# Performance work log

Hardware: AMD Instinct MI355X
Metric: run time of the kernel (lower is better)

The kernel has to match this reference:

```python
import jax, jax.numpy as jnp
import numpy as np

BATCH = 64
EPS = 1e-5
SLOPE = 0.2


def setup_inputs() -> dict:
    key = jax.random.key(0)
    ks = jax.random.split(key, 12)
    def n(k, shape, scale=0.05):
        return jax.random.normal(k, shape, dtype=jnp.float32) * scale
    inp = {"x": jax.random.normal(ks[0], (BATCH, 3, 64, 768), dtype=jnp.float32)}
    depths = [(3, 16), (16, 32), (32, 64), (64, 128), (128, 256)]
    for i, (ci, co) in enumerate(depths):
        inp[f"w{i}"] = n(ks[1 + i], (co, ci, 4, 4))
        inp[f"g{i}"] = jnp.ones((co,), jnp.float32)
        inp[f"b{i}"] = jnp.zeros((co,), jnp.float32)
    inp["w5"] = n(ks[10], (1000, 256, 2, 2))
    inp["lin_w"] = n(ks[11], (64, 1000))
    return inp


def _conv(x, w, s, p):
    return jax.lax.conv_general_dilated(
        x, w, (s, s), ((p, p), (p, p)),
        dimension_numbers=("NCHW", "OIHW", "NCHW"))


def _bn(x, g, b):
    # training-mode BatchNorm2d: batch statistics over (N, H, W)
    m = jnp.mean(x, axis=(0, 2, 3), keepdims=True)
    v = jnp.var(x, axis=(0, 2, 3), keepdims=True)
    return (x - m) * jax.lax.rsqrt(v + EPS) * g[None, :, None, None] + b[None, :, None, None]


def _leaky(x):
    return jnp.where(x >= 0, x, SLOPE * x)


def reference(x, w0, g0, b0, w1, g1, b1, w2, g2, b2, w3, g3, b3, w4, g4, b4, w5, lin_w):
    for w, g, b in [(w0, g0, b0), (w1, g1, b1), (w2, g2, b2), (w3, g3, b3), (w4, g4, b4)]:
        x = _leaky(_bn(_conv(x, w, 2, 1), g, b))
    x = _conv(x, w5, 1, 0)                      # [B, 1000, 1, 23]
    B = x.shape[0]
    sub = x.reshape(B, 1000, -1)                # [B, 1000, 23]
    sub = _leaky(sub)                           # per-slice LeakyReLU == elementwise
    sub = jnp.einsum('bcj,oc->boj', sub, lin_w)  # batched per-slice Linear, fused
    sub = jax.nn.sigmoid(sub)                   # [B, 64, 23]
    a = sub[:, :32, :]                          # low half
    bh = sub[:, 32:, :]                         # high half
    mid = (bh[:, :, :22] + a[:, :, 1:]) * 0.5   # j = 1..22 blend
    small = jnp.concatenate([a[:, :, :1], mid, bh[:, :, 22:]], axis=2)  # [B, 32, 24]
    # torch.cat over dim=1 of small[:,:,j] for j=0..23 -> j-major layout
    return jnp.transpose(small, (0, 2, 1)).reshape(B, 32 * 24)
```

## Files before the change

### kernel.cpp

```cpp
#include <hip/hip_runtime.h>
#include <cmath>

#define EPS 1e-5f
#define SLOPE 0.2f

typedef unsigned short u16;
typedef unsigned int u32;
typedef __attribute__((ext_vector_type(8))) short bf16x8;
typedef __attribute__((ext_vector_type(8))) unsigned short u16x8;
typedef __attribute__((ext_vector_type(4))) unsigned short u16x4;
typedef __attribute__((ext_vector_type(4))) float f32x4;

__device__ __forceinline__ u16 f2b(float f) {
    union { float f; u32 u; } v; v.f = f;
    u32 r = (v.u + 0x7FFF + ((v.u >> 16) & 1)) >> 16;
    return (u16)r;
}
__device__ __forceinline__ float b2f(u16 h) {
    union { u32 u; float f; } v; v.u = ((u32)h) << 16;
    return v.f;
}
__device__ __forceinline__ float leaky(float v) { return v >= 0.f ? v : SLOPE * v; }

__global__ __launch_bounds__(256) void prep(const float* __restrict__ x,
                                            const float* __restrict__ w0,
                                            const float* __restrict__ w1,
                                            const float* __restrict__ w2,
                                            const float* __restrict__ w3,
                                            const float* __restrict__ w4,
                                            const float* __restrict__ w5,
                                            const float* __restrict__ lw,
                                            u16* __restrict__ wbf,
                                            u16* __restrict__ w5b,
                                            u16* __restrict__ lwb,
                                            u16* __restrict__ P) {
    int idx = blockIdx.x * 256 + threadIdx.x;
    if (idx < 697344) {
        const float* src; int K, lgn, base;
        if (idx < 1024)        { src = w0; K = 48;   lgn = 1; base = 0; }
        else if (idx < 9216)   { src = w1; K = 256;  lgn = 3; base = 1024; }
        else if (idx < 41984)  { src = w2; K = 512;  lgn = 4; base = 9216; }
        else if (idx < 173056) { src = w3; K = 1024; lgn = 5; base = 41984; }
        else                   { src = w4; K = 2048; lgn = 6; base = 173056; }
        int local = idx - base;
        int e = local & 7;
        int r = (local >> 3) & 15;
        int q = (local >> 7) & 3;
        int rest = local >> 9;
        int kb = rest & ((1 << lgn) - 1);
        int tm = rest >> lgn;
        int co = tm * 16 + r;
        int k  = kb * 32 + q * 8 + e;
        wbf[idx] = (k < K) ? f2b(src[(size_t)co * K + k]) : (u16)0;
    } else if (idx < 1745920) {
        int local = idx - 697344;
        int k = local & 1023;
        int co = local >> 10;
        w5b[local] = (co < 1000) ? f2b(w5[(size_t)co * 1024 + k]) : (u16)0;
    } else if (idx < 1811456) {
        int local = idx - 1745920;
        int e = local & 7;
        int r = (local >> 3) & 15;
        int q = (local >> 7) & 3;
        int rest = local >> 9;
        int kb = rest & 31;
        int tm = rest >> 5;
        int o = tm * 16 + r;
        int k = kb * 32 + q * 8 + e;
        lwb[local] = (k < 1000) ? f2b(lw[(size_t)o * 1000 + k]) : (u16)0;
    } else if (idx < 3450368) {
        constexpr int H = 64, W = 768, G = 97, Wp = 776, Hp = 66;
        int local = idx - 1811456;
        int m = local % G;
        int hp = (local / G) % Hp;
        int c = (local / (G * Hp)) % 4;
        int b = local / (G * Hp * 4);
        u16x8 o;
#pragma unroll
        for (int i = 0; i < 8; ++i) o[i] = 0;
        if (c < 3 && hp >= 1 && hp <= H) {
            const float* base = x + ((size_t)(b * 3 + c) * H + (hp - 1)) * W;
            if (m > 0) o[0] = f2b(base[8 * m - 1]);
            if (m < G - 1) {
                float4 a  = *(const float4*)(base + 8 * m);
                float4 b4 = *(const float4*)(base + 8 * m + 4);
                o[1] = f2b(a.x); o[2] = f2b(a.y); o[3] = f2b(a.z); o[4] = f2b(a.w);
                o[5] = f2b(b4.x); o[6] = f2b(b4.y); o[7] = f2b(b4.z);
            }
        }
        *(u16x8*)(P + ((size_t)(b * 4 + c) * Hp + hp) * Wp + 8 * m) = o;
    }
}

template <int Co, int CiPad, int Kp, int Hi, int Wi, int Hp, int Wp, int MT, int NT>
__global__ __launch_bounds__(256) void conv_mfma(const u16* __restrict__ inp,
                                                 const u16* __restrict__ wt,
                                                 u16* __restrict__ outb,
                                                 float* __restrict__ part) {
    constexpr int Ho = Hi / 2, Wo = Wi / 2, HW = Ho * Wo;
    constexpr int NTile = 4 * HW;
    constexpr int NG = NTile / NT;
    constexpr int NSLOT = NG / 4;

    int tid = threadIdx.x;
    int wv = tid >> 6;
    int wid = blockIdx.x * 4 + wv;
    int lane = tid & 63;
    int r = lane & 15;
    int quad = lane >> 4;
    int mg = wid / NG;
    int ng = wid % NG;

    int ciq = quad >> 1;
    int kh0 = (quad & 1) * 2;

    const u16* pB[NT];
    int b_[NT], hw_[NT];
#pragma unroll
    for (int i = 0; i < NT; ++i) {
        int n = (ng * NT + i) * 16 + r;
        int b = n / HW;
        int hw = n % HW;
        int oh = hw / Wo;
        int ow = hw % Wo;
        b_[i] = b; hw_[i] = hw;
        pB[i] = inp + ((size_t)(b * CiPad + ciq) * Hp + (2 * oh + kh0)) * Wp + 2 * ow;
    }
    const u16* pA = wt + (size_t)(mg * MT) * 16 * Kp + quad * 128 + r * 8;

    f32x4 acc[MT][NT];
#pragma unroll
    for (int mt = 0; mt < MT; ++mt)
#pragma unroll
        for (int i = 0; i < NT; ++i) acc[mt][i] = (f32x4){0.f, 0.f, 0.f, 0.f};

#pragma unroll 2
    for (int kk = 0; kk < Kp / 32; ++kk) {
        bf16x8 a[MT];
#pragma unroll
        for (int mt = 0; mt < MT; ++mt)
            a[mt] = *(const bf16x8*)(pA + (size_t)mt * 16 * Kp);
#pragma unroll
        for (int i = 0; i < NT; ++i) {
            union { u32 u[4]; bf16x8 v; } bb;
            bb.u[0] = *(const u32*)(pB[i]);
            bb.u[1] = *(const u32*)(pB[i] + 2);
            bb.u[2] = *(const u32*)(pB[i] + Wp);
            bb.u[3] = *(const u32*)(pB[i] + Wp + 2);
#pragma unroll
            for (int mt = 0; mt < MT; ++mt)
                acc[mt][i] = __builtin_amdgcn_mfma_f32_16x16x32_bf16(a[mt], bb.v, acc[mt][i], 0, 0, 0);
            pB[i] += (size_t)2 * Hp * Wp;
        }
        pA += 512;
    }

#pragma unroll
    for (int mt = 0; mt < MT; ++mt) {
        int co0 = mg * MT * 16 + mt * 16 + quad * 4;
#pragma unroll
        for (int i = 0; i < NT; ++i) {
#pragma unroll
            for (int j = 0; j < 4; ++j)
                outb[((size_t)b_[i] * Co + co0 + j) * HW + hw_[i]] = f2b(acc[mt][i][j]);
        }
    }

    __shared__ float sred[4][MT * 16 * 2];
#pragma unroll
    for (int mt = 0; mt < MT; ++mt) {
#pragma unroll
        for (int j = 0; j < 4; ++j) {
            float ls1 = 0.f, ls2 = 0.f;
#pragma unroll
            for (int i = 0; i < NT; ++i) {
                float v = acc[mt][i][j];
                ls1 += v; ls2 += v * v;
            }
#pragma unroll
            for (int m = 1; m < 16; m <<= 1) {
                ls1 += __shfl_xor(ls1, m);
                ls2 += __shfl_xor(ls2, m);
            }
            if (r == 0) {
                int cl = mt * 16 + quad * 4 + j;
                sred[wv][cl * 2 + 0] = ls1;
                sred[wv][cl * 2 + 1] = ls2;
            }
        }
    }
    __syncthreads();
    int slot = blockIdx.x % NSLOT;
    int mgb  = blockIdx.x / NSLOT;
    if (tid < MT * 16) {
        float s1 = (sred[0][tid * 2] + sred[1][tid * 2]) +
                   (sred[2][tid * 2] + sred[3][tid * 2]);
        float s2 = (sred[0][tid * 2 + 1] + sred[1][tid * 2 + 1]) +
                   (sred[2][tid * 2 + 1] + sred[3][tid * 2 + 1]);
        part[((size_t)(mgb * MT * 16 + tid) * NSLOT + slot) * 2 + 0] = s1;
        part[((size_t)(mgb * MT * 16 + tid) * NSLOT + slot) * 2 + 1] = s2;
    }
}

template <int C, int NSLOT>
__global__ __launch_bounds__(256) void bn_finalize_blk(const float* __restrict__ part,
                                                       const float* __restrict__ g,
                                                       const float* __restrict__ bb,
                                                       float* __restrict__ ss, float invN) {
    int c = blockIdx.x;
    int tid = threadIdx.x;
    float s1 = 0.f, s2 = 0.f;
    for (int k = tid; k < NSLOT; k += 256) {
        s1 += part[((size_t)c * NSLOT + k) * 2 + 0];
        s2 += part[((size_t)c * NSLOT + k) * 2 + 1];
    }
    __shared__ float sh1[256], sh2[256];
    sh1[tid] = s1; sh2[tid] = s2;
    __syncthreads();
    for (int s = 128; s > 0; s >>= 1) {
        if (tid < s) { sh1[tid] += sh1[tid + s]; sh2[tid] += sh2[tid + s]; }
        __syncthreads();
    }
    if (tid == 0) {
        float mean = sh1[0] * invN;
        float var  = sh2[0] * invN - mean * mean;
        float inv  = rsqrtf(var + EPS);
        float sc   = inv * g[c];
        ss[c]     = sc;
        ss[C + c] = bb[c] - mean * sc;
    }
}

template <int C, int H, int W>
__global__ __launch_bounds__(256) void bn_pad_v(const u16* __restrict__ in,
                                                const float* __restrict__ ss,
                                                u16* __restrict__ outp) {
    constexpr int G = W / 8 + 1;
    constexpr int Wp = 8 * G;
    constexpr int Hp = H + 2;
    int idx = blockIdx.x * 256 + threadIdx.x;
    if (idx >= 64 * C * Hp * G) return;
    int m = idx % G;
    int hp = (idx / G) % Hp;
    int c = (idx / (G * Hp)) % C;
    int b = idx / (G * Hp * C);

    u16x8 o;
#pragma unroll
    for (int i = 0; i < 8; ++i) o[i] = 0;

    if (hp >= 1 && hp <= H) {
        float sc = ss[c], sh = ss[C + c];
        const u16* base = in + ((size_t)(b * C + c) * H + (hp - 1)) * W;
        if (m > 0) o[0] = f2b(leaky(b2f(base[8 * m - 1]) * sc + sh));
        if (m < G - 1) {
            bf16x8 va = *(const bf16x8*)(base + 8 * m);
#pragma unroll
            for (int i = 0; i < 7; ++i)
                o[i + 1] = f2b(leaky(b2f((u16)va[i]) * sc + sh));
        }
    }
    *(u16x8*)(outp + ((size_t)(b * C + c) * Hp + hp) * Wp + 8 * m) = o;
}

__global__ __launch_bounds__(256) void im2col5(const u16* __restrict__ A,
                                               const float* __restrict__ ss,
                                               u16* __restrict__ ic) {
    int idx = blockIdx.x * 256 + threadIdx.x;
    if (idx >= 1472 * 1024) return;
    int k = idx & 1023;
    int n = idx >> 10;
    int b = n / 23, j = n % 23;
    int ci = k >> 2, kh = (k >> 1) & 1, kw = k & 1;
    float v = b2f(A[(size_t)b * 12288 + ci * 48 + kh * 24 + j + kw]);
    v = leaky(v * ss[ci] + ss[256 + ci]);
    ic[idx] = f2b(v);
}

__global__ __launch_bounds__(256) void conv5_lds(const u16* __restrict__ ic,
                                                 const u16* __restrict__ w5b,
                                                 u16* __restrict__ ic2) {
    __shared__ u16 As[64][72];
    __shared__ u16 Bs[64][72];
    int tid = threadIdx.x;
    int wv = tid >> 6;
    int lane = tid & 63;
    int r = lane & 15;
    int quad = lane >> 4;
    int bid = (blockIdx.x % 8) * 46 + blockIdx.x / 8;
    int gx = bid % 23;
    int gy = bid / 23;

    int trow = tid >> 3;
    int tcol = (tid & 7) * 8;

    f32x4 acc[2][2];
#pragma unroll
    for (int mi = 0; mi < 2; ++mi)
#pragma unroll
        for (int ni = 0; ni < 2; ++ni) acc[mi][ni] = (f32x4){0.f, 0.f, 0.f, 0.f};

    for (int ko = 0; ko < 16; ++ko) {
        int kbase = ko * 64;
        *(bf16x8*)&As[trow][tcol]      = *(const bf16x8*)(w5b + (size_t)(gy * 64 + trow) * 1024 + kbase + tcol);
        *(bf16x8*)&As[trow + 32][tcol] = *(const bf16x8*)(w5b + (size_t)(gy * 64 + trow + 32) * 1024 + kbase + tcol);
        *(bf16x8*)&Bs[trow][tcol]      = *(const bf16x8*)(ic  + (size_t)(gx * 64 + trow) * 1024 + kbase + tcol);
        *(bf16x8*)&Bs[trow + 32][tcol] = *(const bf16x8*)(ic  + (size_t)(gx * 64 + trow + 32) * 1024 + kbase + tcol);
        __syncthreads();
#pragma unroll
        for (int k2 = 0; k2 < 2; ++k2) {
            int koff = k2 * 32 + quad * 8;
            bf16x8 a0 = *(const bf16x8*)&As[(wv >> 1) * 32 + r][koff];
            bf16x8 a1 = *(const bf16x8*)&As[(wv >> 1) * 32 + 16 + r][koff];
            bf16x8 b0 = *(const bf16x8*)&Bs[(wv & 1) * 32 + r][koff];
            bf16x8 b1 = *(const bf16x8*)&Bs[(wv & 1) * 32 + 16 + r][koff];
            acc[0][0] = __builtin_amdgcn_mfma_f32_16x16x32_bf16(a0, b0, acc[0][0], 0, 0, 0);
            acc[0][1] = __builtin_amdgcn_mfma_f32_16x16x32_bf16(a0, b1, acc[0][1], 0, 0, 0);
            acc[1][0] = __builtin_amdgcn_mfma_f32_16x16x32_bf16(a1, b0, acc[1][0], 0, 0, 0);
            acc[1][1] = __builtin_amdgcn_mfma_f32_16x16x32_bf16(a1, b1, acc[1][1], 0, 0, 0);
        }
        __syncthreads();
    }

#pragma unroll
    for (int mi = 0; mi < 2; ++mi) {
#pragma unroll
        for (int ni = 0; ni < 2; ++ni) {
            int n = gx * 64 + (wv & 1) * 32 + ni * 16 + r;
            int co0 = gy * 64 + (wv >> 1) * 32 + mi * 16 + quad * 4;
            u16x4 pk;
#pragma unroll
            for (int j = 0; j < 4; ++j) pk[j] = f2b(leaky(acc[mi][ni][j]));
            *(u16x4*)(ic2 + (size_t)n * 1024 + co0) = pk;
        }
    }
}

__global__ __launch_bounds__(256) void linear_mfma(const u16* __restrict__ ic2,
                                                   const u16* __restrict__ lwb,
                                                   float* __restrict__ sig) {
    int tid = threadIdx.x;
    int wid = blockIdx.x * 4 + (tid >> 6);
    int lane = tid & 63;
    int r = lane & 15;
    int quad = lane >> 4;
    int mt = wid & 3;
    int nt = wid >> 2;

    int n = nt * 16 + r;
    const u16* pA = lwb + (size_t)mt * 16 * 1024 + quad * 128 + r * 8;
    const u16* pB = ic2 + (size_t)n * 1024 + quad * 8;

    f32x4 acc = {0.f, 0.f, 0.f, 0.f};
#pragma unroll 4
    for (int kk = 0; kk < 32; ++kk) {
        bf16x8 a = *(const bf16x8*)pA;
        bf16x8 bv = *(const bf16x8*)pB;
        acc = __builtin_amdgcn_mfma_f32_16x16x32_bf16(a, bv, acc, 0, 0, 0);
        pA += 512;
        pB += 32;
    }

    int b = n / 23, j = n % 23;
#pragma unroll
    for (int jj = 0; jj < 4; ++jj) {
        int o = mt * 16 + quad * 4 + jj;
        float v = 1.f / (1.f + expf(-acc[jj]));
        sig[(size_t)b * 1472 + (size_t)o * 23 + j] = v;
    }
}

__global__ void shuffle_out_kernel(const float* __restrict__ sig, float* __restrict__ out) {
    int idx = blockIdx.x * blockDim.x + threadIdx.x;
    if (idx >= 64 * 768) return;
    int o = idx % 32;
    int j = (idx / 32) % 24;
    int b = idx / 768;
    const float* s = sig + (size_t)b * 64 * 23;
    float v;
    if (j == 0)       v = s[o * 23];
    else if (j == 23) v = s[(o + 32) * 23 + 22];
    else              v = 0.5f * (s[(o + 32) * 23 + (j - 1)] + s[o * 23 + j]);
    out[idx] = v;
}

extern "C" void kernel_launch(void* const* d_in, const int* in_sizes, int n_in,
                              void* d_out, int out_size, void* d_ws, size_t ws_size,
                              hipStream_t stream) {
    (void)in_sizes; (void)n_in; (void)out_size; (void)ws_size;

    const float* x = (const float*)d_in[0];
    const float* w[5]; const float* g[5]; const float* bb[5];
    for (int i = 0; i < 5; ++i) {
        w[i]  = (const float*)d_in[1 + 3 * i];
        g[i]  = (const float*)d_in[2 + 3 * i];
        bb[i] = (const float*)d_in[3 + 3 * i];
    }
    const float* w5 = (const float*)d_in[16];
    const float* lw = (const float*)d_in[17];
    float* out = (float*)d_out;

    float* ws    = (float*)d_ws;
    u16*   A     = (u16*)ws;
    u16*   P     = (u16*)(ws + 6291456);
    u16*   wbf   = (u16*)(ws + 13115392);
    float* ss    = ws + 13472256;
    u16*   w5b   = (u16*)(ws + 13474304);
    u16*   ic    = (u16*)(ws + 13998592);
    u16*   ic2   = (u16*)(ws + 14752256);
    u16*   lwb   = (u16*)(ws + 15505920);
    float* partB = ws + 15538688;
    float* sig   = ws + 4194304;

    const size_t wofs[5] = {0, 1024, 9216, 41984, 173056};

    hipLaunchKernelGGL(prep, dim3(13478), dim3(256), 0, stream,
                       x, w[0], w[1], w[2], w[3], w[4], w5, lw, wbf, w5b, lwb, P);

    hipLaunchKernelGGL((conv_mfma<16, 4, 64, 64, 768, 66, 776, 1, 8>),
                       dim3(1536), dim3(256), 0, stream, P, wbf + wofs[0], A, partB);
    hipLaunchKernelGGL((bn_finalize_blk<16, 1536>), dim3(16), dim3(256), 0, stream,
                       partB, g[0], bb[0], ss, 1.f / 786432.f);
    hipLaunchKernelGGL((bn_pad_v<16, 32, 384>), dim3(6664), dim3(256), 0, stream, A, ss, P);

    hipLaunchKernelGGL((conv_mfma<32, 16, 256, 32, 384, 34, 392, 2, 4>),
                       dim3(768), dim3(256), 0, stream, P, wbf + wofs[1], A, partB);
    hipLaunchKernelGGL((bn_finalize_blk<32, 768>), dim3(32), dim3(256), 0, stream,
                       partB, g[1], bb[1], ss, 1.f / 196608.f);
    hipLaunchKernelGGL((bn_pad_v<32, 16, 192>), dim3(3600), dim3(256), 0, stream, A, ss, P);

    hipLaunchKernelGGL((conv_mfma<64, 32, 512, 16, 192, 18, 200, 4, 2>),
                       dim3(384), dim3(256), 0, stream, P, wbf + wofs[2], A, partB);
    hipLaunchKernelGGL((bn_finalize_blk<64, 384>), dim3(64), dim3(256), 0, stream,
                       partB, g[2], bb[2], ss, 1.f / 49152.f);
    hipLaunchKernelGGL((bn_pad_v<64, 8, 96>), dim3(2080), dim3(256), 0, stream, A, ss, P);

    hipLaunchKernelGGL((conv_mfma<128, 64, 1024, 8, 96, 10, 104, 4, 1>),
                       dim3(384), dim3(256), 0, stream, P, wbf + wofs[3], A, partB);
    hipLaunchKernelGGL((bn_finalize_blk<128, 192>), dim3(128), dim3(256), 0, stream,
                       partB, g[3], bb[3], ss, 1.f / 12288.f);
    hipLaunchKernelGGL((bn_pad_v<128, 4, 48>), dim3(1344), dim3(256), 0, stream, A, ss, P);

    hipLaunchKernelGGL((conv_mfma<256, 128, 2048, 4, 48, 6, 56, 4, 1>),
                       dim3(192), dim3(256), 0, stream, P, wbf + wofs[4], A, partB);
    hipLaunchKernelGGL((bn_finalize_blk<256, 48>), dim3(256), dim3(256), 0, stream,
                       partB, g[4], bb[4], ss, 1.f / 3072.f);
    hipLaunchKernelGGL(im2col5, dim3(5888), dim3(256), 0, stream, A, ss, ic);

    hipLaunchKernelGGL(conv5_lds, dim3(368), dim3(256), 0, stream, ic, w5b, ic2);
    hipLaunchKernelGGL(linear_mfma, dim3(92), dim3(256), 0, stream, ic2, lwb, sig);
    hipLaunchKernelGGL(shuffle_out_kernel, dim3((64 * 768 + 255) / 256), dim3(256), 0, stream,
                       sig, out);
}
```

Before: 178.7 us.

## Fuse BN+LeakyReLU into next conv's operand load, write padded output directly

Each conv now writes its raw bf16 output straight into the interior of a padded buffer. The next conv applies the batch-norm scale/shift and LeakyReLU while loading its B operand, which removes the separate bn_pad pass that read and rewrote every activation. Halo cells are filled with a NaN sentinel by a small halo_fill kernel (or inside prep), and the fused load maps that sentinel back to zero. In exchange, the per-element BN math is redone once for each output that reuses an input pixel, and buffers ping-pong between X and Y.

```diff
diff --git a/kernel.cpp b/kernel.cpp
--- a/kernel.cpp
+++ b/kernel.cpp
@@ -21,6 +21,15 @@
     return v.f;
 }
 __device__ __forceinline__ float leaky(float v) { return v >= 0.f ? v : SLOPE * v; }
+
+__device__ __forceinline__ u32 bnpack(u32 w, float sc, float sh) {
+    union { u32 u; float f; } lo, hi;
+    lo.u = (w & 0xFFFFu) << 16;
+    hi.u = w & 0xFFFF0000u;
+    float tl = lo.f * sc + sh; tl = fmaxf(tl, 0.2f * tl); tl = (lo.f == lo.f) ? tl : 0.f;
+    float th = hi.f * sc + sh; th = fmaxf(th, 0.2f * th); th = (hi.f == hi.f) ? th : 0.f;
+    return ((u32)f2b(tl)) | (((u32)f2b(th)) << 16);
+}
 
 __global__ __launch_bounds__(256) void prep(const float* __restrict__ x,
                                             const float* __restrict__ w0,
@@ -33,7 +42,8 @@
                                             u16* __restrict__ wbf,
                                             u16* __restrict__ w5b,
                                             u16* __restrict__ lwb,
-                                            u16* __restrict__ P) {
+                                            u16* __restrict__ X,
+                                            u16* __restrict__ Y) {
     int idx = blockIdx.x * 256 + threadIdx.x;
     if (idx < 697344) {
         const float* src; int K, lgn, base;
@@ -88,15 +98,42 @@
                 o[5] = f2b(b4.x); o[6] = f2b(b4.y); o[7] = f2b(b4.z);
             }
         }
-        *(u16x8*)(P + ((size_t)(b * 4 + c) * Hp + hp) * Wp + 8 * m) = o;
-    }
-}
-
-template <int Co, int CiPad, int Kp, int Hi, int Wi, int Hp, int Wp, int MT, int NT>
+        *(u16x8*)(X + ((size_t)(b * 4 + c) * Hp + hp) * Wp + 8 * m) = o;
+    } else if (idx < 4515328) {
+        int local = idx - 3450368;
+        int bc = local / 1040;
+        int h = local % 1040;
+        int hp, wp;
+        if (h < 392) { hp = 0; wp = h; }
+        else if (h < 784) { hp = 33; wp = h - 392; }
+        else { int rem = h - 784; int row = rem >> 3; int k = rem & 7; hp = row + 1; wp = (k == 0) ? 0 : 384 + k; }
+        Y[((size_t)bc * 34 + hp) * 392 + wp] = 0x7FC0;
+    }
+}
+
+template <int C, int H, int W>
+__global__ __launch_bounds__(256) void halo_fill(u16* __restrict__ p) {
+    constexpr int Wp = 8 * (W / 8 + 1);
+    constexpr int Hp = H + 2;
+    constexpr int PER = 2 * Wp + 8 * H;
+    int idx = blockIdx.x * 256 + threadIdx.x;
+    if (idx >= 64 * C * PER) return;
+    int bc = idx / PER;
+    int h = idx % PER;
+    int hp, wp;
+    if (h < Wp) { hp = 0; wp = h; }
+    else if (h < 2 * Wp) { hp = H + 1; wp = h - Wp; }
+    else { int rem = h - 2 * Wp; int row = rem >> 3; int k = rem & 7; hp = row + 1; wp = (k == 0) ? 0 : W + k; }
+    p[((size_t)bc * Hp + hp) * Wp + wp] = 0x7FC0;
+}
+
+template <int Co, int CiPad, int Kp, int Hi, int Wi, int Hp, int Wp, int MT, int NT,
+          bool INBN, int HpO, int WpO>
 __global__ __launch_bounds__(256) void conv_mfma(const u16* __restrict__ inp,
                                                  const u16* __restrict__ wt,
                                                  u16* __restrict__ outb,
-                                                 float* __restrict__ part) {
+                                                 float* __restrict__ part,
+                                                 const float* __restrict__ ssin) {
     constexpr int Ho = Hi / 2, Wo = Wi / 2, HW = Ho * Wo;
     constexpr int NTile = 4 * HW;
     constexpr int NG = NTile / NT;
@@ -115,7 +152,7 @@
     int kh0 = (quad & 1) * 2;
 
     const u16* pB[NT];
-    int b_[NT], hw_[NT];
+    int b_[NT], oh_[NT], ow_[NT];
 #pragma unroll
     for (int i = 0; i < NT; ++i) {
         int n = (ng * NT + i) * 16 + r;
@@ -123,7 +160,7 @@
         int hw = n % HW;
         int oh = hw / Wo;
         int ow = hw % Wo;
-        b_[i] = b; hw_[i] = hw;
+        b_[i] = b; oh_[i] = oh; ow_[i] = ow;
         pB[i] = inp + ((size_t)(b * CiPad + ciq) * Hp + (2 * oh + kh0)) * Wp + 2 * ow;
     }
     const u16* pA = wt + (size_t)(mg * MT) * 16 * Kp + quad * 128 + r * 8;
@@ -140,13 +177,27 @@
 #pragma unroll
         for (int mt = 0; mt < MT; ++mt)
             a[mt] = *(const bf16x8*)(pA + (size_t)mt * 16 * Kp);
+        float sc = 0.f, sh = 0.f;
+        if (INBN) {
+            int ci = kk * 2 + ciq;
+            sc = ssin[ci];
+            sh = ssin[CiPad + ci];
+        }
 #pragma unroll
         for (int i = 0; i < NT; ++i) {
             union { u32 u[4]; bf16x8 v; } bb;
-            bb.u[0] = *(const u32*)(pB[i]);
-            bb.u[1] = *(const u32*)(pB[i] + 2);
-            bb.u[2] = *(const u32*)(pB[i] + Wp);
-            bb.u[3] = *(const u32*)(pB[i] + Wp + 2);
+            u32 r0 = *(const u32*)(pB[i]);
+            u32 r1 = *(const u32*)(pB[i] + 2);
+            u32 r2 = *(const u32*)(pB[i] + Wp);
+            u32 r3 = *(const u32*)(pB[i] + Wp + 2);
+            if (INBN) {
+                bb.u[0] = bnpack(r0, sc, sh);
+                bb.u[1] = bnpack(r1, sc, sh);
+                bb.u[2] = bnpack(r2, sc, sh);
+                bb.u[3] = bnpack(r3, sc, sh);
+            } else {
+                bb.u[0] = r0; bb.u[1] = r1; bb.u[2] = r2; bb.u[3] = r3;
+            }
 #pragma unroll
             for (int mt = 0; mt < MT; ++mt)
                 acc[mt][i] = __builtin_amdgcn_mfma_f32_16x16x32_bf16(a[mt], bb.v, acc[mt][i], 0, 0, 0);
@@ -160,9 +211,17 @@
         int co0 = mg * MT * 16 + mt * 16 + quad * 4;
 #pragma unroll
         for (int i = 0; i < NT; ++i) {
-#pragma unroll
-            for (int j = 0; j < 4; ++j)
-                outb[((size_t)b_[i] * Co + co0 + j) * HW + hw_[i]] = f2b(acc[mt][i][j]);
+            if (HpO > 0) {
+#pragma unroll
+                for (int j = 0; j < 4; ++j)
+                    outb[((size_t)(b_[i] * Co + co0 + j) * HpO + oh_[i] + 1) * WpO + ow_[i] + 1]
+                        = f2b(acc[mt][i][j]);
+            } else {
+                int hw = oh_[i] * Wo + ow_[i];
+#pragma unroll
+                for (int j = 0; j < 4; ++j)
+                    outb[((size_t)b_[i] * Co + co0 + j) * HW + hw] = f2b(acc[mt][i][j]);
+            }
         }
     }
 
@@ -229,38 +288,6 @@
         ss[c]     = sc;
         ss[C + c] = bb[c] - mean * sc;
     }
-}
-
-template <int C, int H, int W>
-__global__ __launch_bounds__(256) void bn_pad_v(const u16* __restrict__ in,
-                                                const float* __restrict__ ss,
-                                                u16* __restrict__ outp) {
-    constexpr int G = W / 8 + 1;
-    constexpr int Wp = 8 * G;
-    constexpr int Hp = H + 2;
-    int idx = blockIdx.x * 256 + threadIdx.x;
-    if (idx >= 64 * C * Hp * G) return;
-    int m = idx % G;
-    int hp = (idx / G) % Hp;
-    int c = (idx / (G * Hp)) % C;
-    int b = idx / (G * Hp * C);
-
-    u16x8 o;
-#pragma unroll
-    for (int i = 0; i < 8; ++i) o[i] = 0;
-
-    if (hp >= 1 && hp <= H) {
-        float sc = ss[c], sh = ss[C + c];
-        const u16* base = in + ((size_t)(b * C + c) * H + (hp - 1)) * W;
-        if (m > 0) o[0] = f2b(leaky(b2f(base[8 * m - 1]) * sc + sh));
-        if (m < G - 1) {
-            bf16x8 va = *(const bf16x8*)(base + 8 * m);
-#pragma unroll
-            for (int i = 0; i < 7; ++i)
-                o[i + 1] = f2b(leaky(b2f((u16)va[i]) * sc + sh));
-        }
-    }
-    *(u16x8*)(outp + ((size_t)(b * C + c) * Hp + hp) * Wp + 8 * m) = o;
 }
 
 __global__ __launch_bounds__(256) void im2col5(const u16* __restrict__ A,
@@ -401,48 +428,48 @@
     float* out = (float*)d_out;
 
     float* ws    = (float*)d_ws;
-    u16*   A     = (u16*)ws;
-    u16*   P     = (u16*)(ws + 6291456);
-    u16*   wbf   = (u16*)(ws + 13115392);
-    float* ss    = ws + 13472256;
-    u16*   w5b   = (u16*)(ws + 13474304);
-    u16*   ic    = (u16*)(ws + 13998592);
-    u16*   ic2   = (u16*)(ws + 14752256);
-    u16*   lwb   = (u16*)(ws + 15505920);
-    float* partB = ws + 15538688;
-    float* sig   = ws + 4194304;
+    u16*   X     = (u16*)ws;
+    u16*   Y     = (u16*)(ws + 6555648);
+    u16*   A     = (u16*)(ws + 13379584);
+    u16*   wbf   = (u16*)(ws + 13772800);
+    u16*   w5b   = (u16*)(ws + 14121472);
+    u16*   lwb   = (u16*)(ws + 14645760);
+    u16*   ic    = (u16*)(ws + 14678528);
+    u16*   ic2   = (u16*)(ws + 15432192);
+    float* ss    = ws + 16185856;
+    float* partB = ws + 16186368;
+    float* sig   = ws + 16284672;
 
     const size_t wofs[5] = {0, 1024, 9216, 41984, 173056};
 
-    hipLaunchKernelGGL(prep, dim3(13478), dim3(256), 0, stream,
-                       x, w[0], w[1], w[2], w[3], w[4], w5, lw, wbf, w5b, lwb, P);
-
-    hipLaunchKernelGGL((conv_mfma<16, 4, 64, 64, 768, 66, 776, 1, 8>),
-                       dim3(1536), dim3(256), 0, stream, P, wbf + wofs[0], A, partB);
+    hipLaunchKernelGGL(prep, dim3(17638), dim3(256), 0, stream,
+                       x, w[0], w[1], w[2], w[3], w[4], w5, lw, wbf, w5b, lwb, X, Y);
+
+    hipLaunchKernelGGL((conv_mfma<16, 4, 64, 64, 768, 66, 776, 1, 8, false, 34, 392>),
+                       dim3(1536), dim3(256), 0, stream, X, wbf + wofs[0], Y, partB, ss);
     hipLaunchKernelGGL((bn_finalize_blk<16, 1536>), dim3(16), dim3(256), 0, stream,
                        partB, g[0], bb[0], ss, 1.f / 786432.f);
-    hipLaunchKernelGGL((bn_pad_v<16, 32, 384>), dim3(6664), dim3(256), 0, stream, A, ss, P);
-
-    hipLaunchKernelGGL((conv_mfma<32, 16, 256, 32, 384, 34, 392, 2, 4>),
-                       dim3(768), dim3(256), 0, stream, P, wbf + wofs[1], A, partB);
+    hipLaunchKernelGGL((halo_fill<32, 16, 192>), dim3(4224), dim3(256), 0, stream, X);
+
+    hipLaunchKernelGGL((conv_mfma<32, 16, 256, 32, 384, 34, 392, 2, 4, true, 18, 200>),
+                       dim3(768), dim3(256), 0, stream, Y, wbf + wofs[1], X, partB, ss);
     hipLaunchKernelGGL((bn_finalize_blk<32, 768>), dim3(32), dim3(256), 0, stream,
                        partB, g[1], bb[1], ss, 1.f / 196608.f);
-    hipLaunchKernelGGL((bn_pad_v<32, 16, 192>), dim3(3600), dim3(256), 0, stream, A, ss, P);
-
-    hipLaunchKernelGGL((conv_mfma<64, 32, 512, 16, 192, 18, 200, 4, 2>),
-                       dim3(384), dim3(256), 0, stream, P, wbf + wofs[2], A, partB);
+    hipLaunchKernelGGL((halo_fill<64, 8, 96>), dim3(4352), dim3(256), 0, stream, Y);
+
+    hipLaunchKernelGGL((conv_mfma<64, 32, 512, 16, 192, 18, 200, 4, 2, true, 10, 104>),
+                       dim3(384), dim3(256), 0, stream, X, wbf + wofs[2], Y, partB, ss);
     hipLaunchKernelGGL((bn_finalize_blk<64, 384>), dim3(64), dim3(256), 0, stream,
                        partB, g[2], bb[2], ss, 1.f / 49152.f);
-    hipLaunchKernelGGL((bn_pad_v<64, 8, 96>), dim3(2080), dim3(256), 0, stream, A, ss, P);
-
-    hipLaunchKernelGGL((conv_mfma<128, 64, 1024, 8, 96, 10, 104, 4, 1>),
-                       dim3(384), dim3(256), 0, stream, P, wbf + wofs[3], A, partB);
+    hipLaunchKernelGGL((halo_fill<128, 4, 48>), dim3(4608), dim3(256), 0, stream, X);
+
+    hipLaunchKernelGGL((conv_mfma<128, 64, 1024, 8, 96, 10, 104, 4, 1, true, 6, 56>),
+                       dim3(384), dim3(256), 0, stream, Y, wbf + wofs[3], X, partB, ss);
     hipLaunchKernelGGL((bn_finalize_blk<128, 192>), dim3(128), dim3(256), 0, stream,
                        partB, g[3], bb[3], ss, 1.f / 12288.f);
-    hipLaunchKernelGGL((bn_pad_v<128, 4, 48>), dim3(1344), dim3(256), 0, stream, A, ss, P);
-
-    hipLaunchKernelGGL((conv_mfma<256, 128, 2048, 4, 48, 6, 56, 4, 1>),
-                       dim3(192), dim3(256), 0, stream, P, wbf + wofs[4], A, partB);
+
+    hipLaunchKernelGGL((conv_mfma<256, 128, 2048, 4, 48, 6, 56, 4, 1, true, 0, 0>),
+                       dim3(192), dim3(256), 0, stream, X, wbf + wofs[4], A, partB, ss);
     hipLaunchKernelGGL((bn_finalize_blk<256, 48>), dim3(256), dim3(256), 0, stream,
                        partB, g[4], bb[4], ss, 1.f / 3072.f);
     hipLaunchKernelGGL(im2col5, dim3(5888), dim3(256), 0, stream, A, ss, ic);
```

Result: slower. 184.0 us (+3.0%).
